# Performance work log

Measured on AMD Instinct MI355X. Metric: run time of the kernel, lower is better.

Reference implementation:

```python
import jax, jax.numpy as jnp
import numpy as np

B, C, D, W, H = 4, 256, 32, 32, 32  # img_dim = D, in_channels = C, model_num = 4


def setup_inputs() -> dict:
    key = jax.random.key(0)
    ks = jax.random.split(key, 8)
    s = 0.02
    inp = {
        "m1": jax.random.normal(ks[0], (B, C, D, W, H), jnp.float32),
        "m2": jax.random.normal(ks[1], (B, C, D, W, H), jnp.float32),
        "m3": jax.random.normal(ks[2], (B, C, D, W, H), jnp.float32),
        "m4": jax.random.normal(ks[3], (B, C, D, W, H), jnp.float32),
        # nn.Linear weights (torch convention: y = x @ W.T + b)
        "Wq": jax.random.normal(ks[4], (D, D), jnp.float32) * s,
        "bq": jnp.zeros((D,), jnp.float32),
        "Wk": jax.random.normal(ks[5], (D, D), jnp.float32) * s,
        "bk": jnp.zeros((D,), jnp.float32),
        # four 1x1x1 Conv3d kernels, squeezed to [model, out_c, in_c]
        "Wc": jax.random.normal(ks[6], (4, C, C), jnp.float32) * s,
        "bc": jnp.zeros((4, C), jnp.float32),
    }
    return inp


def reference(m1, m2, m3, m4, Wq, bq, Wk, bk, Wc, bc):
    d = m1.shape[2]
    # adaptive_avg_pool3d(x, (D,1,1)) == mean over W,H -> [B,C,D]; stack 4 modalities -> [B,C,4,D]
    pooled = jnp.stack([m.mean(axis=(3, 4)) for m in (m1, m2, m3, m4)], axis=2)
    q = jnp.einsum('bcd,ed->bce', pooled[:, :, 0], Wq) + bq          # [B,C,D]
    k = jnp.einsum('bcmd,ed->bcme', pooled, Wk) + bk                 # [B,C,4,D]
    # per-modality attention logits: q . k_m over D -> [B,C,4]
    a = jnp.einsum('bcd,bcmd->bcm', q, k) / jnp.sqrt(jnp.float32(d))
    a = jax.nn.softmax(a, axis=-1)                                   # [B,C,4]
    ms = jnp.stack([m1, m2, m3, m4], axis=0)                         # [4,B,C,D,W,H]
    # 1x1x1 Conv3d == channel-mixing GEMM per voxel
    conv = jnp.einsum('mbcdwh,moc->mbodwh', ms, Wc) + bc[:, None, :, None, None, None]
    # weighted sum of the 4 conv outputs by per-(B,C) attention weights
    out = jnp.einsum('bcm,mbcdwh->bcdwh', a, conv)                   # [B,C,D,W,H]
    return out
```

## Files before the change

### kernel.cpp

```cpp
#include <hip/hip_runtime.h>
#include <hip/hip_bf16.h>

#define NB 4
#define NC 256
#define ND 32
#define WH 1024
#define DWH 32768
#define KTOT 1024

typedef __attribute__((ext_vector_type(8))) short short8;
typedef __attribute__((ext_vector_type(4))) float f32x4;

static __device__ __forceinline__ unsigned short f32_to_bf16(float f) {
    unsigned u = __builtin_bit_cast(unsigned, f);
    u = u + 0x7fff + ((u >> 16) & 1);
    return (unsigned short)(u >> 16);
}

static __device__ __forceinline__ unsigned pack_bf16x2(float lo, float hi) {
    return (unsigned)f32_to_bf16(lo) | ((unsigned)f32_to_bf16(hi) << 16);
}

__global__ __launch_bounds__(256) void pool_kernel(
    const float* __restrict__ i0, const float* __restrict__ i1,
    const float* __restrict__ i2, const float* __restrict__ i3,
    float* __restrict__ pooled)
{
    int bid = blockIdx.x;
    int m   = bid & 3;
    int bc  = bid >> 2;
    const float* src = (m == 0 ? i0 : m == 1 ? i1 : m == 2 ? i2 : i3)
                       + (size_t)bc * DWH;
    int t = threadIdx.x;
    int wave = t >> 6, lane = t & 63;

    for (int d = wave; d < ND; d += 4) {
        const float4* row = (const float4*)(src + (size_t)d * WH);
        float s = 0.f;
        #pragma unroll
        for (int j = 0; j < 4; ++j) {
            float4 v = row[lane + 64 * j];
            s += v.x + v.y + v.z + v.w;
        }
        #pragma unroll
        for (int off = 32; off; off >>= 1) s += __shfl_down(s, off, 64);
        if (lane == 0) pooled[bc * 128 + m * 32 + d] = s * (1.0f / 1024.0f);
    }
}

__global__ __launch_bounds__(64) void attn_kernel(
    const float* __restrict__ pooled,
    const float* __restrict__ Wq, const float* __restrict__ bq,
    const float* __restrict__ Wk, const float* __restrict__ bk,
    const float* __restrict__ Wc, const float* __restrict__ bcv,
    unsigned short* __restrict__ Amat, float* __restrict__ beff)
{
    int bc_idx = blockIdx.x;
    int lane = threadIdx.x;
    int e = lane & 31;
    const float* P = pooled + bc_idx * 128;

    float q = 0.f, kv[4] = {0.f, 0.f, 0.f, 0.f};
    for (int d = 0; d < 32; ++d) {
        float pq = P[d];
        float wq = Wq[e * 32 + d], wk = Wk[e * 32 + d];
        q += pq * wq;
        #pragma unroll
        for (int m = 0; m < 4; ++m) kv[m] += P[m * 32 + d] * wk;
    }
    q += bq[e];
    #pragma unroll
    for (int m = 0; m < 4; ++m) kv[m] += bk[e];

    float lg[4];
    #pragma unroll
    for (int m = 0; m < 4; ++m) {
        float p = q * kv[m];
        #pragma unroll
        for (int off = 16; off; off >>= 1) p += __shfl_xor(p, off, 32);
        lg[m] = p * 0.17677669529663687f;
    }
    float mx = fmaxf(fmaxf(lg[0], lg[1]), fmaxf(lg[2], lg[3]));
    float ex[4], s = 0.f;
    #pragma unroll
    for (int m = 0; m < 4; ++m) { ex[m] = __expf(lg[m] - mx); s += ex[m]; }
    float a[4];
    #pragma unroll
    for (int m = 0; m < 4; ++m) a[m] = ex[m] / s;

    int c = bc_idx & 255;
    if (lane == 0) {
        float be = 0.f;
        #pragma unroll
        for (int m = 0; m < 4; ++m) be += a[m] * bcv[m * NC + c];
        beff[bc_idx] = be;
    }
    unsigned short* Arow = Amat + (size_t)bc_idx * KTOT;
    #pragma unroll
    for (int j = 0; j < 16; ++j) {
        int k = j * 64 + lane;
        int m = k >> 8, cin = k & 255;
        float v = a[m] * Wc[(m * NC + c) * NC + cin];
        Arow[k] = f32_to_bf16(v);
    }
}

#define BM 128
#define BN 128
#define BK 64

static __device__ __forceinline__ int swz(int row, int chunk) {
    return row * 64 + ((chunk ^ (row & 7)) << 3);
}

__global__ __launch_bounds__(256, 2) void gemm_kernel(
    const float* __restrict__ i0, const float* __restrict__ i1,
    const float* __restrict__ i2, const float* __restrict__ i3,
    const unsigned short* __restrict__ Amat,
    const float* __restrict__ beff,
    float* __restrict__ out)
{
    __shared__ __align__(16) short As[2 * BM * BK];
    __shared__ __align__(16) short Bs[2 * BN * BK];

    int raw = blockIdx.x;
    int sb  = (raw & 7) * 256 + (raw >> 3);
    int ot = sb & 1;
    int xt = (sb >> 1) & 255;
    int b  = sb >> 9;
    int o0 = ot * BM, x0 = xt * BN;

    const unsigned short* Ab = Amat + ((size_t)b * NC + o0) * KTOT;

    int t = threadIdx.x;
    int wave = t >> 6, lane = t & 63;
    int wr = wave >> 1, wc = wave & 1;
    int lrow = lane & 15, lk = lane >> 4;

    f32x4 acc[4][4];
    #pragma unroll
    for (int mi = 0; mi < 4; ++mi)
        #pragma unroll
        for (int ni = 0; ni < 4; ++ni)
            acc[mi][ni] = (f32x4){0.f, 0.f, 0.f, 0.f};

    int xq = t & 31;
    int kb = (t >> 5) * 8;

    int ar = wave * 32 + (lane >> 3);
    int aq = (lane & 7) ^ (lane >> 3);
    const unsigned short* asrc = Ab + (size_t)ar * KTOT + aq * 8;

    float4 v[8];

    {
        const float* Bb = i0 + (size_t)b * NC * DWH + x0;
        #pragma unroll
        for (int j = 0; j < 8; ++j)
            v[j] = *(const float4*)(Bb + (size_t)(kb + j) * DWH + xq * 4);
        #pragma unroll
        for (int p = 0; p < 4; ++p)
            __builtin_amdgcn_global_load_lds(
                (const __attribute__((address_space(1))) unsigned int*)
                    (asrc + (size_t)p * 8 * KTOT),
                (__attribute__((address_space(3))) unsigned int*)
                    (As + (wave * 32 + p * 8) * 64),
                16, 0, 0);
        __builtin_amdgcn_sched_barrier(0);
        uint4 pk[4];
        #pragma unroll
        for (int i = 0; i < 4; ++i) {
            unsigned w[4];
            #pragma unroll
            for (int j = 0; j < 4; ++j)
                w[j] = pack_bf16x2(((const float*)&v[2 * j])[i],
                                   ((const float*)&v[2 * j + 1])[i]);
            pk[i] = (uint4){w[0], w[1], w[2], w[3]};
        }
        const float* Bb1 = i0 + ((size_t)b * NC + 64) * DWH + x0;
        #pragma unroll
        for (int j = 0; j < 8; ++j)
            v[j] = *(const float4*)(Bb1 + (size_t)(kb + j) * DWH + xq * 4);
        __builtin_amdgcn_sched_barrier(0);
        #pragma unroll
        for (int i = 0; i < 4; ++i)
            *(uint4*)(&Bs[swz(xq * 4 + i, t >> 5)]) = pk[i];
        asm volatile("s_waitcnt vmcnt(8) lgkmcnt(0)" ::: "memory");
        __builtin_amdgcn_s_barrier();
        __builtin_amdgcn_sched_barrier(0);
    }

    int cur = 0;
    for (int it = 0; it < KTOT / BK; ++it) {
        int itn  = (it < 15) ? it + 1 : 15;
        int itn2 = (it < 14) ? it + 2 : 15;
        short* Asw = As + (cur ^ 1) * (BM * BK);
        short* Bsw = Bs + (cur ^ 1) * (BN * BK);

        #pragma unroll
        for (int p = 0; p < 4; ++p)
            __builtin_amdgcn_global_load_lds(
                (const __attribute__((address_space(1))) unsigned int*)
                    (asrc + (size_t)p * 8 * KTOT + itn * BK),
                (__attribute__((address_space(3))) unsigned int*)
                    (Asw + (wave * 32 + p * 8) * 64),
                16, 0, 0);
        __builtin_amdgcn_sched_barrier(0);

        uint4 pk[4];
        #pragma unroll
        for (int i = 0; i < 4; ++i) {
            unsigned w[4];
            #pragma unroll
            for (int j = 0; j < 4; ++j)
                w[j] = pack_bf16x2(((const float*)&v[2 * j])[i],
                                   ((const float*)&v[2 * j + 1])[i]);
            pk[i] = (uint4){w[0], w[1], w[2], w[3]};
        }

        {
            int m = itn2 >> 2, cbase = (itn2 & 3) * 64;
            const float* Bb = (m == 0 ? i0 : m == 1 ? i1 : m == 2 ? i2 : i3)
                              + ((size_t)b * NC + cbase) * DWH + x0;
            #pragma unroll
            for (int j = 0; j < 8; ++j)
                v[j] = *(const float4*)(Bb + (size_t)(kb + j) * DWH + xq * 4);
        }
        __builtin_amdgcn_sched_barrier(0);

        #pragma unroll
        for (int i = 0; i < 4; ++i)
            *(uint4*)(&Bsw[swz(xq * 4 + i, t >> 5)]) = pk[i];

        const short* Asr = As + cur * (BM * BK);
        const short* Bsr = Bs + cur * (BN * BK);
        #pragma unroll
        for (int kk = 0; kk < 2; ++kk) {
            int q = kk * 4 + lk;
            short8 af[4], bf[4];
            #pragma unroll
            for (int mi = 0; mi < 4; ++mi) {
                int r = wr * 64 + mi * 16 + lrow;
                af[mi] = *(const short8*)(&Asr[swz(r, q)]);
            }
            #pragma unroll
            for (int ni = 0; ni < 4; ++ni) {
                int x = wc * 64 + ni * 16 + lrow;
                bf[ni] = *(const short8*)(&Bsr[swz(x, q)]);
            }
            __builtin_amdgcn_s_setprio(1);
            #pragma unroll
            for (int mi = 0; mi < 4; ++mi)
                #pragma unroll
                for (int ni = 0; ni < 4; ++ni)
                    acc[mi][ni] = __builtin_amdgcn_mfma_f32_16x16x32_bf16(
                        af[mi], bf[ni], acc[mi][ni], 0, 0, 0);
            __builtin_amdgcn_s_setprio(0);
        }

        asm volatile("s_waitcnt vmcnt(8) lgkmcnt(0)" ::: "memory");
        __builtin_amdgcn_s_barrier();
        __builtin_amdgcn_sched_barrier(0);
        cur ^= 1;
    }

    const float* beff_b = beff + b * NC + o0;
    float* outb = out + ((size_t)b * NC + o0) * DWH + x0;
    #pragma unroll
    for (int mi = 0; mi < 4; ++mi) {
        #pragma unroll
        for (int r4 = 0; r4 < 4; ++r4) {
            int row = wr * 64 + mi * 16 + lk * 4 + r4;
            float bias = beff_b[row];
            float* orow = outb + (size_t)row * DWH;
            #pragma unroll
            for (int ni = 0; ni < 4; ++ni) {
                int col = wc * 64 + ni * 16 + lrow;
                orow[col] = acc[mi][ni][r4] + bias;
            }
        }
    }
}

extern "C" void kernel_launch(void* const* d_in, const int* in_sizes, int n_in,
                              void* d_out, int out_size, void* d_ws, size_t ws_size,
                              hipStream_t stream) {
    const float* m1 = (const float*)d_in[0];
    const float* m2 = (const float*)d_in[1];
    const float* m3 = (const float*)d_in[2];
    const float* m4 = (const float*)d_in[3];
    const float* Wq = (const float*)d_in[4];
    const float* bq = (const float*)d_in[5];
    const float* Wk = (const float*)d_in[6];
    const float* bk = (const float*)d_in[7];
    const float* Wc = (const float*)d_in[8];
    const float* bcv = (const float*)d_in[9];
    float* out = (float*)d_out;

    float* pooled        = (float*)d_ws;
    unsigned short* Amat = (unsigned short*)((char*)d_ws + 524288);
    float* beff          = (float*)((char*)d_ws + 524288 + 2097152);

    pool_kernel<<<NB * NC * 4, 256, 0, stream>>>(m1, m2, m3, m4, pooled);
    attn_kernel<<<NB * NC, 64, 0, stream>>>(pooled, Wq, bq, Wk, bk, Wc, bcv,
                                            Amat, beff);
    gemm_kernel<<<(NB) * (NC / BM) * (DWH / BN), 256, 0, stream>>>(
        m1, m2, m3, m4, Amat, beff, out);
}
```

Baseline: 267.5 us.

## Load A fragments directly from global into registers, drop A LDS staging

The A (attention-scaled weight) tiles are no longer staged through LDS with global_load_lds. Each wave now loads its MFMA A fragments straight from global memory into registers every iteration. This halves LDS use so the launch bound can rise to three blocks per CU, and it removes the A LDS traffic. In exchange the A loads are issued in the same iteration they are consumed, so their global latency is exposed, and the explicit vmcnt waits and several sched_barriers are removed, which may change how loads overlap with compute.

```diff
diff --git a/kernel.cpp b/kernel.cpp
--- a/kernel.cpp
+++ b/kernel.cpp
@@ -113,14 +113,13 @@
     return row * 64 + ((chunk ^ (row & 7)) << 3);
 }
 
-__global__ __launch_bounds__(256, 2) void gemm_kernel(
+__global__ __launch_bounds__(256, 3) void gemm_kernel(
     const float* __restrict__ i0, const float* __restrict__ i1,
     const float* __restrict__ i2, const float* __restrict__ i3,
     const unsigned short* __restrict__ Amat,
     const float* __restrict__ beff,
     float* __restrict__ out)
 {
-    __shared__ __align__(16) short As[2 * BM * BK];
     __shared__ __align__(16) short Bs[2 * BN * BK];
 
     int raw = blockIdx.x;
@@ -137,6 +136,8 @@
     int wr = wave >> 1, wc = wave & 1;
     int lrow = lane & 15, lk = lane >> 4;
 
+    const unsigned short* Abase = Ab + (size_t)(wr * 64 + lrow) * KTOT + lk * 8;
+
     f32x4 acc[4][4];
     #pragma unroll
     for (int mi = 0; mi < 4; ++mi)
@@ -147,10 +148,6 @@
     int xq = t & 31;
     int kb = (t >> 5) * 8;
 
-    int ar = wave * 32 + (lane >> 3);
-    int aq = (lane & 7) ^ (lane >> 3);
-    const unsigned short* asrc = Ab + (size_t)ar * KTOT + aq * 8;
-
     float4 v[8];
 
     {
@@ -158,15 +155,6 @@
         #pragma unroll
         for (int j = 0; j < 8; ++j)
             v[j] = *(const float4*)(Bb + (size_t)(kb + j) * DWH + xq * 4);
-        #pragma unroll
-        for (int p = 0; p < 4; ++p)
-            __builtin_amdgcn_global_load_lds(
-                (const __attribute__((address_space(1))) unsigned int*)
-                    (asrc + (size_t)p * 8 * KTOT),
-                (__attribute__((address_space(3))) unsigned int*)
-                    (As + (wave * 32 + p * 8) * 64),
-                16, 0, 0);
-        __builtin_amdgcn_sched_barrier(0);
         uint4 pk[4];
         #pragma unroll
         for (int i = 0; i < 4; ++i) {
@@ -181,31 +169,24 @@
         #pragma unroll
         for (int j = 0; j < 8; ++j)
             v[j] = *(const float4*)(Bb1 + (size_t)(kb + j) * DWH + xq * 4);
-        __builtin_amdgcn_sched_barrier(0);
         #pragma unroll
         for (int i = 0; i < 4; ++i)
             *(uint4*)(&Bs[swz(xq * 4 + i, t >> 5)]) = pk[i];
-        asm volatile("s_waitcnt vmcnt(8) lgkmcnt(0)" ::: "memory");
+        asm volatile("s_waitcnt lgkmcnt(0)" ::: "memory");
         __builtin_amdgcn_s_barrier();
         __builtin_amdgcn_sched_barrier(0);
     }
 
     int cur = 0;
+    #pragma unroll 1
     for (int it = 0; it < KTOT / BK; ++it) {
-        int itn  = (it < 15) ? it + 1 : 15;
-        int itn2 = (it < 14) ? it + 2 : 15;
-        short* Asw = As + (cur ^ 1) * (BM * BK);
-        short* Bsw = Bs + (cur ^ 1) * (BN * BK);
-
-        #pragma unroll
-        for (int p = 0; p < 4; ++p)
-            __builtin_amdgcn_global_load_lds(
-                (const __attribute__((address_space(1))) unsigned int*)
-                    (asrc + (size_t)p * 8 * KTOT + itn * BK),
-                (__attribute__((address_space(3))) unsigned int*)
-                    (Asw + (wave * 32 + p * 8) * 64),
-                16, 0, 0);
-        __builtin_amdgcn_sched_barrier(0);
+        short8 af0[4], af1[4];
+        #pragma unroll
+        for (int mi = 0; mi < 4; ++mi) {
+            const unsigned short* ap = Abase + (size_t)mi * 16 * KTOT + it * BK;
+            af0[mi] = *(const short8*)(ap);
+            af1[mi] = *(const short8*)(ap + 32);
+        }
 
         uint4 pk[4];
         #pragma unroll
@@ -219,6 +200,7 @@
         }
 
         {
+            int itn2 = (it < 14) ? it + 2 : 15;
             int m = itn2 >> 2, cbase = (itn2 & 3) * 64;
             const float* Bb = (m == 0 ? i0 : m == 1 ? i1 : m == 2 ? i2 : i3)
                               + ((size_t)b * NC + cbase) * DWH + x0;
@@ -226,23 +208,17 @@
             for (int j = 0; j < 8; ++j)
                 v[j] = *(const float4*)(Bb + (size_t)(kb + j) * DWH + xq * 4);
         }
-        __builtin_amdgcn_sched_barrier(0);
-
+
+        short* Bsw = Bs + (cur ^ 1) * (BN * BK);
         #pragma unroll
         for (int i = 0; i < 4; ++i)
             *(uint4*)(&Bsw[swz(xq * 4 + i, t >> 5)]) = pk[i];
 
-        const short* Asr = As + cur * (BM * BK);
         const short* Bsr = Bs + cur * (BN * BK);
         #pragma unroll
         for (int kk = 0; kk < 2; ++kk) {
             int q = kk * 4 + lk;
-            short8 af[4], bf[4];
-            #pragma unroll
-            for (int mi = 0; mi < 4; ++mi) {
-                int r = wr * 64 + mi * 16 + lrow;
-                af[mi] = *(const short8*)(&Asr[swz(r, q)]);
-            }
+            short8 bf[4];
             #pragma unroll
             for (int ni = 0; ni < 4; ++ni) {
                 int x = wc * 64 + ni * 16 + lrow;
@@ -250,15 +226,17 @@
             }
             __builtin_amdgcn_s_setprio(1);
             #pragma unroll
-            for (int mi = 0; mi < 4; ++mi)
+            for (int mi = 0; mi < 4; ++mi) {
+                short8 a = kk ? af1[mi] : af0[mi];
                 #pragma unroll
                 for (int ni = 0; ni < 4; ++ni)
                     acc[mi][ni] = __builtin_amdgcn_mfma_f32_16x16x32_bf16(
-                        af[mi], bf[ni], acc[mi][ni], 0, 0, 0);
+                        a, bf[ni], acc[mi][ni], 0, 0, 0);
+            }
             __builtin_amdgcn_s_setprio(0);
         }
 
-        asm volatile("s_waitcnt vmcnt(8) lgkmcnt(0)" ::: "memory");
+        asm volatile("s_waitcnt lgkmcnt(0)" ::: "memory");
         __builtin_amdgcn_s_barrier();
         __builtin_amdgcn_sched_barrier(0);
         cur ^= 1;
```

Measured after the change: 718.9 us. 169% more time.
